# Optimization experiments

Measured on AMD Instinct MI355X. Metric: run time of the kernel, lower is better.

Reference implementation:

```python
import jax, jax.numpy as jnp
import numpy as np

RHO = 1.0
MU = 1e-05
DT = 1.0 / 32
DX = 1.0 / 255
DY = 1.0 / 255


def _residuals(x, std):
    # x: [B, 3, H, W]; torch does x *= std (pure version here)
    x = x * std
    u = x[:, 0]  # [B, H, W]
    v = x[:, 1]
    p = x[:, 2]
    r = jnp.roll

    dudt = (r(u, -1, 0) - r(u, 1, 0)) / DT
    dvdt = (r(v, -1, 0) - r(v, 1, 0)) / DT
    dudx = (r(u, -1, 1) - r(u, 1, 1)) / (2 * DX)
    dudy = (r(u, -1, 2) - r(u, 1, 2)) / (2 * DY)
    dvdx = (r(v, -1, 1) - r(v, 1, 1)) / (2 * DX)
    dvdy = (r(v, -1, 2) - r(v, 1, 2)) / (2 * DY)
    dpdx = (r(p, -1, 1) - r(p, 1, 1)) / (2 * DX)
    dpdy = (r(p, -1, 2) - r(p, 1, 2)) / (2 * DY)
    d2udx2 = (r(u, -1, 1) - 2 * u + r(u, 1, 1)) / DX ** 2
    d2udy2 = (r(u, -1, 2) - 2 * u + r(u, 1, 2)) / DY ** 2
    d2vdx2 = (r(v, -1, 1) - 2 * v + r(v, 1, 1)) / DX ** 2
    d2vdy2 = (r(v, -1, 2) - 2 * v + r(v, 1, 2)) / DY ** 2

    t = lambda a: a[1:-1, 1:-1, 1:-1]  # trim periodic-wrap halo
    u, v = t(u), t(v)
    r0 = jnp.abs(t(dudx) + t(dvdy))
    r1 = jnp.abs(RHO * (t(dudt) + u * t(dudx) + v * t(dudy)) + t(dpdx)
                 - MU * (t(d2udx2) + t(d2udy2)))
    r2 = jnp.abs(RHO * (t(dvdt) + u * t(dvdx) + v * t(dvdy)) + t(dpdy)
                 - MU * (t(d2vdx2) + t(d2vdy2)))
    return r0, r1, r2


def setup_inputs() -> dict:
    key = jax.random.key(0)
    k1, k2, k3 = jax.random.split(key, 3)
    B, C, H, W = 64, 3, 512, 512
    x = jax.random.normal(k1, (B, C, H, W), dtype=jnp.float32)
    y = jax.random.normal(k2, (B, C, H, W), dtype=jnp.float32)
    std = jax.random.uniform(k3, (), dtype=jnp.float32)
    return {"x": x, "y": y, "std": std}


def reference(x, y, std):
    r0_y, r1_y, r2_y = _residuals(y, std)
    r0_x, r1_x, r2_x = _residuals(x, std)
    d0 = jnp.mean((r0_y - r0_x) ** 2)
    d1 = jnp.mean((r1_y - r1_x) ** 2)
    d2 = jnp.mean((r2_y - r2_x) ** 2)
    return 0.001 * (d0 + d1 + d2)
```

## Files before the change

### kernel.cpp

```cpp
#include <hip/hip_runtime.h>


constexpr int Wd   = 512;
constexpr int CSTR = 512 * 512;
constexpr int BSTR = 3 * 512 * 512;

__device__ __forceinline__ float4 ld4(const float* p) {
    return *reinterpret_cast<const float4*>(p);
}
__device__ __forceinline__ float4 scale4(float4 a, float s) {
    return make_float4(a.x * s, a.y * s, a.z * s, a.w * s);
}

__device__ __forceinline__ void plane_resid(
    const float (&L)[3][4][256],
    int io, int jt, int jl,
    float4 eu, float4 ev, float4 ep,
    float4 um, float4 uc, float4 un,
    float4 vm, float4 vc, float4 vn,
    float4 pc,
    float uL, float vL, float pL,
    float uR, float vR, float pR,
    float sdx,
    float r0[4], float r1[4], float r2[4])
{
    float4 uxm, vxm, pxm, uxp, vxp, pxp;
    if (io == 0) { uxm = eu; vxm = ev; pxm = ep; }
    else {
        uxm = ld4(&L[0][io - 1][jl]);
        vxm = ld4(&L[1][io - 1][jl]);
        pxm = ld4(&L[2][io - 1][jl]);
    }
    if (io == 3) { uxp = eu; vxp = ev; pxp = ep; }
    else {
        uxp = ld4(&L[0][io + 1][jl]);
        vxp = ld4(&L[1][io + 1][jl]);
        pxp = ld4(&L[2][io + 1][jl]);
    }

    float u_l = __shfl_up(uc.w, 1);
    float v_l = __shfl_up(vc.w, 1);
    float p_l = __shfl_up(pc.w, 1);
    float u_r = __shfl_down(uc.x, 1);
    float v_r = __shfl_down(vc.x, 1);
    float p_r = __shfl_down(pc.x, 1);
    if (jt == 0)  { u_l = uL; v_l = vL; p_l = pL; }
    if (jt == 63) { u_r = uR; v_r = vR; p_r = pR; }

    const float ucA[4] = {uc.x, uc.y, uc.z, uc.w};
    const float vcA[4] = {vc.x, vc.y, vc.z, vc.w};
    const float umA[4] = {um.x, um.y, um.z, um.w};
    const float vmA[4] = {vm.x, vm.y, vm.z, vm.w};
    const float unA[4] = {un.x, un.y, un.z, un.w};
    const float vnA[4] = {vn.x, vn.y, vn.z, vn.w};
    const float ul[4]  = {u_l, uc.x, uc.y, uc.z};
    const float ur[4]  = {uc.y, uc.z, uc.w, u_r};
    const float vl[4]  = {v_l, vc.x, vc.y, vc.z};
    const float vr[4]  = {vc.y, vc.z, vc.w, v_r};
    const float pl[4]  = {p_l, pc.x, pc.y, pc.z};
    const float pr[4]  = {pc.y, pc.z, pc.w, p_r};
    const float uxpA[4] = {uxp.x, uxp.y, uxp.z, uxp.w};
    const float uxmA[4] = {uxm.x, uxm.y, uxm.z, uxm.w};
    const float vxpA[4] = {vxp.x, vxp.y, vxp.z, vxp.w};
    const float vxmA[4] = {vxm.x, vxm.y, vxm.z, vxm.w};
    const float pxpA[4] = {pxp.x, pxp.y, pxp.z, pxp.w};
    const float pxmA[4] = {pxm.x, pxm.y, pxm.z, pxm.w};

    #pragma unroll
    for (int k = 0; k < 4; ++k) {
        const float dudx = (uxpA[k] - uxmA[k]) * 127.5f;
        const float dvdx = (vxpA[k] - vxmA[k]) * 127.5f;
        const float dpdx = (pxpA[k] - pxmA[k]) * sdx;
        const float dudy = (ur[k] - ul[k]) * 127.5f;
        const float dvdy = (vr[k] - vl[k]) * 127.5f;
        const float dpdy = (pr[k] - pl[k]) * sdx;
        const float lapu = (uxpA[k] + uxmA[k] + ur[k] + ul[k]) * 0.65025f
                         - 2.601f * ucA[k];
        const float lapv = (vxpA[k] + vxmA[k] + vr[k] + vl[k]) * 0.65025f
                         - 2.601f * vcA[k];
        r0[k] = fabsf(dudx + dvdy);
        r1[k] = fabsf((unA[k] - umA[k]) * 32.0f + ucA[k] * dudx + vcA[k] * dudy
                      + dpdx - lapu);
        r2[k] = fabsf((vnA[k] - vmA[k]) * 32.0f + ucA[k] * dvdx + vcA[k] * dvdy
                      + dpdy - lapv);
    }
}

__global__ __launch_bounds__(256)
void ns_loss_kernel(const float* __restrict__ X, const float* __restrict__ Y,
                    const float* __restrict__ stdp, double* __restrict__ acc)
{
    __shared__ float lds[2][2][3][4][256];
    __shared__ float smr[3][4];

    const float s   = *stdp;
    const float sdx = s * 127.5f;

    const int orig = blockIdx.x;
    const int grp  = orig & 7;
    const int band = orig >> 3;
    const int z    = grp >> 1;
    const int jh   = grp & 1;

    const int tid = threadIdx.x;
    const int io  = tid >> 6;
    const int jt  = tid & 63;
    const int jl  = jt << 2;
    const int j0g = (jh << 8) + jl;
    const int irow = 1 + band * 4 + io;
    const int i    = min(irow, 511);
    const bool vrow = (irow <= 510);
    const int bs = 1 + 15 * z + (z == 3 ? 1 : 0);
    const int nsteps = (z < 2) ? 15 : 16;

    int c = bs * BSTR + i * Wd + j0g;
    const int eoff = (io == 0) ? -Wd : ((i < 511) ? Wd : 0);
    const bool isedge = (io == 0) || (io == 3);
    const int offL = (j0g == 0) ? 0 : -1;
    const int offR = (j0g == 508) ? 3 : 4;

    float4 xum = scale4(ld4(X + c - BSTR), s);
    float4 xuc = scale4(ld4(X + c), s);
    float4 xun = scale4(ld4(X + c + BSTR), s);
    float4 xvm = scale4(ld4(X + c - BSTR + CSTR), s);
    float4 xvc = scale4(ld4(X + c + CSTR), s);
    float4 xvn = scale4(ld4(X + c + BSTR + CSTR), s);
    float4 xpc = ld4(X + c + 2 * CSTR);
    float4 xpn = ld4(X + c + 2 * CSTR + BSTR);
    float4 yum = scale4(ld4(Y + c - BSTR), s);
    float4 yuc = scale4(ld4(Y + c), s);
    float4 yun = scale4(ld4(Y + c + BSTR), s);
    float4 yvm = scale4(ld4(Y + c - BSTR + CSTR), s);
    float4 yvc = scale4(ld4(Y + c + CSTR), s);
    float4 yvn = scale4(ld4(Y + c + BSTR + CSTR), s);
    float4 ypc = ld4(Y + c + 2 * CSTR);
    float4 ypn = ld4(Y + c + 2 * CSTR + BSTR);

    *(float4*)&lds[0][0][0][io][jl] = xuc;
    *(float4*)&lds[0][0][1][io][jl] = xvc;
    *(float4*)&lds[0][0][2][io][jl] = xpc;
    *(float4*)&lds[0][1][0][io][jl] = yuc;
    *(float4*)&lds[0][1][1][io][jl] = yvc;
    *(float4*)&lds[0][1][2][io][jl] = ypc;
    __syncthreads();

    float s0 = 0.0f, s1 = 0.0f, s2 = 0.0f;

    for (int k = 0; k < nsteps; ++k) {
        const int cur = k & 1;

        float4 xeu = make_float4(0, 0, 0, 0), xev = xeu, xep = xeu;
        float4 yeu = xeu, yev = xeu, yep = xeu;
        if (isedge) {
            xeu = scale4(ld4(X + c + eoff), s);
            xev = scale4(ld4(X + c + CSTR + eoff), s);
            xep = ld4(X + c + 2 * CSTR + eoff);
            yeu = scale4(ld4(Y + c + eoff), s);
            yev = scale4(ld4(Y + c + CSTR + eoff), s);
            yep = ld4(Y + c + 2 * CSTR + eoff);
        }
        float xuL = 0, xvL = 0, xpL = 0, yuL = 0, yvL = 0, ypL = 0;
        float xuR = 0, xvR = 0, xpR = 0, yuR = 0, yvR = 0, ypR = 0;
        if (jt == 0) {
            xuL = X[c + offL] * s; xvL = X[c + CSTR + offL] * s;
            xpL = X[c + 2 * CSTR + offL];
            yuL = Y[c + offL] * s; yvL = Y[c + CSTR + offL] * s;
            ypL = Y[c + 2 * CSTR + offL];
        }
        if (jt == 63) {
            xuR = X[c + offR] * s; xvR = X[c + CSTR + offR] * s;
            xpR = X[c + 2 * CSTR + offR];
            yuR = Y[c + offR] * s; yvR = Y[c + CSTR + offR] * s;
            ypR = Y[c + 2 * CSTR + offR];
        }

        float r0x[4], r1x[4], r2x[4], r0y[4], r1y[4], r2y[4];
        plane_resid(lds[cur][0], io, jt, jl, xeu, xev, xep,
                    xum, xuc, xun, xvm, xvc, xvn, xpc,
                    xuL, xvL, xpL, xuR, xvR, xpR, sdx, r0x, r1x, r2x);
        plane_resid(lds[cur][1], io, jt, jl, yeu, yev, yep,
                    yum, yuc, yun, yvm, yvc, yvn, ypc,
                    yuL, yvL, ypL, yuR, yvR, ypR, sdx, r0y, r1y, r2y);

        #pragma unroll
        for (int kk = 0; kk < 4; ++kk) {
            float e0 = r0y[kk] - r0x[kk];
            float e1 = r1y[kk] - r1x[kk];
            float e2 = r2y[kk] - r2x[kk];
            const bool dead = (!vrow) || (kk == 0 && j0g == 0)
                                      || (kk == 3 && j0g == 508);
            if (dead) { e0 = 0.0f; e1 = 0.0f; e2 = 0.0f; }
            s0 += e0 * e0; s1 += e1 * e1; s2 += e2 * e2;
        }

        *(float4*)&lds[cur ^ 1][0][0][io][jl] = xun;
        *(float4*)&lds[cur ^ 1][0][1][io][jl] = xvn;
        *(float4*)&lds[cur ^ 1][0][2][io][jl] = xpn;
        *(float4*)&lds[cur ^ 1][1][0][io][jl] = yun;
        *(float4*)&lds[cur ^ 1][1][1][io][jl] = yvn;
        *(float4*)&lds[cur ^ 1][1][2][io][jl] = ypn;

        const int pfo = (k + 1 < nsteps) ? 2 * BSTR : BSTR;
        const float4 xu2 = scale4(ld4(X + c + pfo), s);
        const float4 xv2 = scale4(ld4(X + c + pfo + CSTR), s);
        const float4 xp2 = ld4(X + c + pfo + 2 * CSTR);
        const float4 yu2 = scale4(ld4(Y + c + pfo), s);
        const float4 yv2 = scale4(ld4(Y + c + pfo + CSTR), s);
        const float4 yp2 = ld4(Y + c + pfo + 2 * CSTR);

        xum = xuc; xuc = xun; xun = xu2;
        xvm = xvc; xvc = xvn; xvn = xv2;
        xpc = xpn; xpn = xp2;
        yum = yuc; yuc = yun; yun = yu2;
        yvm = yvc; yvc = yvn; yvn = yv2;
        ypc = ypn; ypn = yp2;

        asm volatile("s_waitcnt lgkmcnt(0)" ::: "memory");
        __builtin_amdgcn_s_barrier();
        c += BSTR;
    }

    for (int o = 32; o > 0; o >>= 1) {
        s0 += __shfl_down(s0, o);
        s1 += __shfl_down(s1, o);
        s2 += __shfl_down(s2, o);
    }
    const int wid = tid >> 6;
    if (jt == 0) { smr[0][wid] = s0; smr[1][wid] = s1; smr[2][wid] = s2; }
    __syncthreads();
    if (tid == 0) {
        atomicAdd(&acc[0], (double)smr[0][0] + (double)smr[0][1]
                         + (double)smr[0][2] + (double)smr[0][3]);
        atomicAdd(&acc[1], (double)smr[1][0] + (double)smr[1][1]
                         + (double)smr[1][2] + (double)smr[1][3]);
        atomicAdd(&acc[2], (double)smr[2][0] + (double)smr[2][1]
                         + (double)smr[2][2] + (double)smr[2][3]);
    }
}

__global__ void ns_finalize_kernel(const double* __restrict__ acc,
                                   float* __restrict__ out)
{
    if (threadIdx.x == 0) {
        const double N = 62.0 * 510.0 * 510.0;
        out[0] = (float)(1.0e-3 * (acc[0] + acc[1] + acc[2]) / N);
    }
}

extern "C" void kernel_launch(void* const* d_in, const int* in_sizes, int n_in,
                              void* d_out, int out_size, void* d_ws, size_t ws_size,
                              hipStream_t stream) {
    const float* X    = (const float*)d_in[0];
    const float* Y    = (const float*)d_in[1];
    const float* stdp = (const float*)d_in[2];
    float* out  = (float*)d_out;
    double* acc = (double*)d_ws;

    hipMemsetAsync(acc, 0, 3 * sizeof(double), stream);

    dim3 block(256);
    dim3 grid(1024);
    ns_loss_kernel<<<grid, block, 0, stream>>>(X, Y, stdp, acc);
    ns_finalize_kernel<<<1, 64, 0, stream>>>(acc, out);
}
```

Baseline: 136.6 us.

## Split batch into five chunks, drop pressure LDS staging, remap block order

The grid grows from 1024 to 1280 blocks by cutting the batch dimension into five chunks of 12-13 steps instead of four chunks of 15-16. Block indices are remapped so that adjacent blocks cover different z chunks. The pressure channel is no longer staged in LDS; its row neighbours are read directly from global memory each step, which shrinks LDS and may raise occupancy. The shared reduction scratch now reuses the LDS buffer. The cost is more redundant halo loads per step, and the pressure neighbour loads may read one row before or after the valid rows on boundary bands.

```diff
diff --git a/kernel.cpp b/kernel.cpp
--- a/kernel.cpp
+++ b/kernel.cpp
@@ -13,29 +13,27 @@
 }
 
 __device__ __forceinline__ void plane_resid(
-    const float (&L)[3][4][256],
+    const float (&L)[2][4][256],
     int io, int jt, int jl,
-    float4 eu, float4 ev, float4 ep,
+    float4 eu, float4 ev,
     float4 um, float4 uc, float4 un,
     float4 vm, float4 vc, float4 vn,
-    float4 pc,
+    float4 pc, float4 pxp4, float4 pxm4,
     float uL, float vL, float pL,
     float uR, float vR, float pR,
     float sdx,
     float r0[4], float r1[4], float r2[4])
 {
-    float4 uxm, vxm, pxm, uxp, vxp, pxp;
-    if (io == 0) { uxm = eu; vxm = ev; pxm = ep; }
+    float4 uxm, vxm, uxp, vxp;
+    if (io == 0) { uxm = eu; vxm = ev; }
     else {
         uxm = ld4(&L[0][io - 1][jl]);
         vxm = ld4(&L[1][io - 1][jl]);
-        pxm = ld4(&L[2][io - 1][jl]);
-    }
-    if (io == 3) { uxp = eu; vxp = ev; pxp = ep; }
+    }
+    if (io == 3) { uxp = eu; vxp = ev; }
     else {
         uxp = ld4(&L[0][io + 1][jl]);
         vxp = ld4(&L[1][io + 1][jl]);
-        pxp = ld4(&L[2][io + 1][jl]);
     }
 
     float u_l = __shfl_up(uc.w, 1);
@@ -63,8 +61,8 @@
     const float uxmA[4] = {uxm.x, uxm.y, uxm.z, uxm.w};
     const float vxpA[4] = {vxp.x, vxp.y, vxp.z, vxp.w};
     const float vxmA[4] = {vxm.x, vxm.y, vxm.z, vxm.w};
-    const float pxpA[4] = {pxp.x, pxp.y, pxp.z, pxp.w};
-    const float pxmA[4] = {pxm.x, pxm.y, pxm.z, pxm.w};
+    const float pxpA[4] = {pxp4.x, pxp4.y, pxp4.z, pxp4.w};
+    const float pxmA[4] = {pxm4.x, pxm4.y, pxm4.z, pxm4.w};
 
     #pragma unroll
     for (int k = 0; k < 4; ++k) {
@@ -90,17 +88,17 @@
 void ns_loss_kernel(const float* __restrict__ X, const float* __restrict__ Y,
                     const float* __restrict__ stdp, double* __restrict__ acc)
 {
-    __shared__ float lds[2][2][3][4][256];
-    __shared__ float smr[3][4];
+    __shared__ float lds[2][2][2][4][256];
 
     const float s   = *stdp;
     const float sdx = s * 127.5f;
 
     const int orig = blockIdx.x;
-    const int grp  = orig & 7;
-    const int band = orig >> 3;
-    const int z    = grp >> 1;
-    const int jh   = grp & 1;
+    const int wg   = (orig & 7) * 160 + (orig >> 3);
+    const int z    = wg >> 8;
+    const int rem  = wg & 255;
+    const int jh   = rem >> 7;
+    const int band = rem & 127;
 
     const int tid = threadIdx.x;
     const int io  = tid >> 6;
@@ -110,8 +108,8 @@
     const int irow = 1 + band * 4 + io;
     const int i    = min(irow, 511);
     const bool vrow = (irow <= 510);
-    const int bs = 1 + 15 * z + (z == 3 ? 1 : 0);
-    const int nsteps = (z < 2) ? 15 : 16;
+    const int bs     = (z < 2) ? (1 + 13 * z) : (27 + 12 * (z - 2));
+    const int nsteps = (z < 2) ? 13 : 12;
 
     int c = bs * BSTR + i * Wd + j0g;
     const int eoff = (io == 0) ? -Wd : ((i < 511) ? Wd : 0);
@@ -126,7 +124,6 @@
     float4 xvc = scale4(ld4(X + c + CSTR), s);
     float4 xvn = scale4(ld4(X + c + BSTR + CSTR), s);
     float4 xpc = ld4(X + c + 2 * CSTR);
-    float4 xpn = ld4(X + c + 2 * CSTR + BSTR);
     float4 yum = scale4(ld4(Y + c - BSTR), s);
     float4 yuc = scale4(ld4(Y + c), s);
     float4 yun = scale4(ld4(Y + c + BSTR), s);
@@ -134,14 +131,13 @@
     float4 yvc = scale4(ld4(Y + c + CSTR), s);
     float4 yvn = scale4(ld4(Y + c + BSTR + CSTR), s);
     float4 ypc = ld4(Y + c + 2 * CSTR);
+    float4 xpn = ld4(X + c + 2 * CSTR + BSTR);
     float4 ypn = ld4(Y + c + 2 * CSTR + BSTR);
 
     *(float4*)&lds[0][0][0][io][jl] = xuc;
     *(float4*)&lds[0][0][1][io][jl] = xvc;
-    *(float4*)&lds[0][0][2][io][jl] = xpc;
     *(float4*)&lds[0][1][0][io][jl] = yuc;
     *(float4*)&lds[0][1][1][io][jl] = yvc;
-    *(float4*)&lds[0][1][2][io][jl] = ypc;
     __syncthreads();
 
     float s0 = 0.0f, s1 = 0.0f, s2 = 0.0f;
@@ -149,15 +145,17 @@
     for (int k = 0; k < nsteps; ++k) {
         const int cur = k & 1;
 
-        float4 xeu = make_float4(0, 0, 0, 0), xev = xeu, xep = xeu;
-        float4 yeu = xeu, yev = xeu, yep = xeu;
+        const float4 xpxp = ld4(X + c + 2 * CSTR + Wd);
+        const float4 xpxm = ld4(X + c + 2 * CSTR - Wd);
+        const float4 ypxp = ld4(Y + c + 2 * CSTR + Wd);
+        const float4 ypxm = ld4(Y + c + 2 * CSTR - Wd);
+        float4 xeu = make_float4(0, 0, 0, 0), xev = xeu;
+        float4 yeu = xeu, yev = xeu;
         if (isedge) {
             xeu = scale4(ld4(X + c + eoff), s);
             xev = scale4(ld4(X + c + CSTR + eoff), s);
-            xep = ld4(X + c + 2 * CSTR + eoff);
             yeu = scale4(ld4(Y + c + eoff), s);
             yev = scale4(ld4(Y + c + CSTR + eoff), s);
-            yep = ld4(Y + c + 2 * CSTR + eoff);
         }
         float xuL = 0, xvL = 0, xpL = 0, yuL = 0, yvL = 0, ypL = 0;
         float xuR = 0, xvR = 0, xpR = 0, yuR = 0, yvR = 0, ypR = 0;
@@ -175,11 +173,11 @@
         }
 
         float r0x[4], r1x[4], r2x[4], r0y[4], r1y[4], r2y[4];
-        plane_resid(lds[cur][0], io, jt, jl, xeu, xev, xep,
-                    xum, xuc, xun, xvm, xvc, xvn, xpc,
+        plane_resid(lds[cur][0], io, jt, jl, xeu, xev,
+                    xum, xuc, xun, xvm, xvc, xvn, xpc, xpxp, xpxm,
                     xuL, xvL, xpL, xuR, xvR, xpR, sdx, r0x, r1x, r2x);
-        plane_resid(lds[cur][1], io, jt, jl, yeu, yev, yep,
-                    yum, yuc, yun, yvm, yvc, yvn, ypc,
+        plane_resid(lds[cur][1], io, jt, jl, yeu, yev,
+                    yum, yuc, yun, yvm, yvc, yvn, ypc, ypxp, ypxm,
                     yuL, yvL, ypL, yuR, yvR, ypR, sdx, r0y, r1y, r2y);
 
         #pragma unroll
@@ -195,10 +193,8 @@
 
         *(float4*)&lds[cur ^ 1][0][0][io][jl] = xun;
         *(float4*)&lds[cur ^ 1][0][1][io][jl] = xvn;
-        *(float4*)&lds[cur ^ 1][0][2][io][jl] = xpn;
         *(float4*)&lds[cur ^ 1][1][0][io][jl] = yun;
         *(float4*)&lds[cur ^ 1][1][1][io][jl] = yvn;
-        *(float4*)&lds[cur ^ 1][1][2][io][jl] = ypn;
 
         const int pfo = (k + 1 < nsteps) ? 2 * BSTR : BSTR;
         const float4 xu2 = scale4(ld4(X + c + pfo), s);
@@ -225,16 +221,17 @@
         s1 += __shfl_down(s1, o);
         s2 += __shfl_down(s2, o);
     }
+    float* red = &lds[0][0][0][0][0];
     const int wid = tid >> 6;
-    if (jt == 0) { smr[0][wid] = s0; smr[1][wid] = s1; smr[2][wid] = s2; }
+    if (jt == 0) { red[wid] = s0; red[4 + wid] = s1; red[8 + wid] = s2; }
     __syncthreads();
     if (tid == 0) {
-        atomicAdd(&acc[0], (double)smr[0][0] + (double)smr[0][1]
-                         + (double)smr[0][2] + (double)smr[0][3]);
-        atomicAdd(&acc[1], (double)smr[1][0] + (double)smr[1][1]
-                         + (double)smr[1][2] + (double)smr[1][3]);
-        atomicAdd(&acc[2], (double)smr[2][0] + (double)smr[2][1]
-                         + (double)smr[2][2] + (double)smr[2][3]);
+        atomicAdd(&acc[0], (double)red[0] + (double)red[1]
+                         + (double)red[2] + (double)red[3]);
+        atomicAdd(&acc[1], (double)red[4] + (double)red[5]
+                         + (double)red[6] + (double)red[7]);
+        atomicAdd(&acc[2], (double)red[8] + (double)red[9]
+                         + (double)red[10] + (double)red[11]);
     }
 }
 
@@ -259,7 +256,7 @@
     hipMemsetAsync(acc, 0, 3 * sizeof(double), stream);
 
     dim3 block(256);
-    dim3 grid(1024);
+    dim3 grid(1280);
     ns_loss_kernel<<<grid, block, 0, stream>>>(X, Y, stdp, acc);
     ns_finalize_kernel<<<1, 64, 0, stream>>>(acc, out);
 }
```

New measurement: 161.8 us. +18.5%, slower.

## Split X and Y residual work across two thread groups in 512-thread blocks

Applied to the files above, without the earlier changes.

Doubles the block to 512 threads so one half computes residuals for X and the other for Y, with the X residuals exchanged through shared memory for the squared-difference sum. Each thread now holds roughly half the register state, which is meant to raise occupancy and memory-level parallelism. The one-step-ahead register prefetch with a double-buffered LDS stage is replaced by a single stage buffer loaded inside the loop, and a second barrier per step is added for the exchange. This risks exposing more load latency and adds synchronisation overhead.

```diff
diff --git a/kernel.cpp b/kernel.cpp
--- a/kernel.cpp
+++ b/kernel.cpp
@@ -86,11 +86,12 @@
     }
 }
 
-__global__ __launch_bounds__(256)
+__global__ __launch_bounds__(512)
 void ns_loss_kernel(const float* __restrict__ X, const float* __restrict__ Y,
                     const float* __restrict__ stdp, double* __restrict__ acc)
 {
-    __shared__ float lds[2][2][3][4][256];
+    __shared__ float stage[2][3][4][256];
+    __shared__ float rxch[3][4][256];
     __shared__ float smr[3][4];
 
     const float s   = *stdp;
@@ -103,8 +104,10 @@
     const int jh   = grp & 1;
 
     const int tid = threadIdx.x;
-    const int io  = tid >> 6;
-    const int jt  = tid & 63;
+    const int tg  = tid >> 8;
+    const int t8  = tid & 255;
+    const int io  = t8 >> 6;
+    const int jt  = t8 & 63;
     const int jl  = jt << 2;
     const int j0g = (jh << 8) + jl;
     const int irow = 1 + band * 4 + io;
@@ -113,120 +116,91 @@
     const int bs = 1 + 15 * z + (z == 3 ? 1 : 0);
     const int nsteps = (z < 2) ? 15 : 16;
 
+    const float* __restrict__ T = tg ? Y : X;
     int c = bs * BSTR + i * Wd + j0g;
     const int eoff = (io == 0) ? -Wd : ((i < 511) ? Wd : 0);
     const bool isedge = (io == 0) || (io == 3);
     const int offL = (j0g == 0) ? 0 : -1;
     const int offR = (j0g == 508) ? 3 : 4;
 
-    float4 xum = scale4(ld4(X + c - BSTR), s);
-    float4 xuc = scale4(ld4(X + c), s);
-    float4 xun = scale4(ld4(X + c + BSTR), s);
-    float4 xvm = scale4(ld4(X + c - BSTR + CSTR), s);
-    float4 xvc = scale4(ld4(X + c + CSTR), s);
-    float4 xvn = scale4(ld4(X + c + BSTR + CSTR), s);
-    float4 xpc = ld4(X + c + 2 * CSTR);
-    float4 xpn = ld4(X + c + 2 * CSTR + BSTR);
-    float4 yum = scale4(ld4(Y + c - BSTR), s);
-    float4 yuc = scale4(ld4(Y + c), s);
-    float4 yun = scale4(ld4(Y + c + BSTR), s);
-    float4 yvm = scale4(ld4(Y + c - BSTR + CSTR), s);
-    float4 yvc = scale4(ld4(Y + c + CSTR), s);
-    float4 yvn = scale4(ld4(Y + c + BSTR + CSTR), s);
-    float4 ypc = ld4(Y + c + 2 * CSTR);
-    float4 ypn = ld4(Y + c + 2 * CSTR + BSTR);
-
-    *(float4*)&lds[0][0][0][io][jl] = xuc;
-    *(float4*)&lds[0][0][1][io][jl] = xvc;
-    *(float4*)&lds[0][0][2][io][jl] = xpc;
-    *(float4*)&lds[0][1][0][io][jl] = yuc;
-    *(float4*)&lds[0][1][1][io][jl] = yvc;
-    *(float4*)&lds[0][1][2][io][jl] = ypc;
-    __syncthreads();
+    float4 um = scale4(ld4(T + c - BSTR), s);
+    float4 uc = scale4(ld4(T + c), s);
+    float4 vm = scale4(ld4(T + c - BSTR + CSTR), s);
+    float4 vc = scale4(ld4(T + c + CSTR), s);
+    float4 pc = ld4(T + c + 2 * CSTR);
 
     float s0 = 0.0f, s1 = 0.0f, s2 = 0.0f;
 
     for (int k = 0; k < nsteps; ++k) {
-        const int cur = k & 1;
-
-        float4 xeu = make_float4(0, 0, 0, 0), xev = xeu, xep = xeu;
-        float4 yeu = xeu, yev = xeu, yep = xeu;
+        const float4 unr = ld4(T + c + BSTR);
+        const float4 vnr = ld4(T + c + BSTR + CSTR);
+        const float4 pn  = ld4(T + c + BSTR + 2 * CSTR);
+        float4 eu = uc, ev = vc, ep = pc;
         if (isedge) {
-            xeu = scale4(ld4(X + c + eoff), s);
-            xev = scale4(ld4(X + c + CSTR + eoff), s);
-            xep = ld4(X + c + 2 * CSTR + eoff);
-            yeu = scale4(ld4(Y + c + eoff), s);
-            yev = scale4(ld4(Y + c + CSTR + eoff), s);
-            yep = ld4(Y + c + 2 * CSTR + eoff);
-        }
-        float xuL = 0, xvL = 0, xpL = 0, yuL = 0, yvL = 0, ypL = 0;
-        float xuR = 0, xvR = 0, xpR = 0, yuR = 0, yvR = 0, ypR = 0;
+            eu = scale4(ld4(T + c + eoff), s);
+            ev = scale4(ld4(T + c + CSTR + eoff), s);
+            ep = ld4(T + c + 2 * CSTR + eoff);
+        }
+        float uL = 0, vL = 0, pL = 0, uR = 0, vR = 0, pR = 0;
         if (jt == 0) {
-            xuL = X[c + offL] * s; xvL = X[c + CSTR + offL] * s;
-            xpL = X[c + 2 * CSTR + offL];
-            yuL = Y[c + offL] * s; yvL = Y[c + CSTR + offL] * s;
-            ypL = Y[c + 2 * CSTR + offL];
+            uL = T[c + offL] * s; vL = T[c + CSTR + offL] * s;
+            pL = T[c + 2 * CSTR + offL];
         }
         if (jt == 63) {
-            xuR = X[c + offR] * s; xvR = X[c + CSTR + offR] * s;
-            xpR = X[c + 2 * CSTR + offR];
-            yuR = Y[c + offR] * s; yvR = Y[c + CSTR + offR] * s;
-            ypR = Y[c + 2 * CSTR + offR];
-        }
-
-        float r0x[4], r1x[4], r2x[4], r0y[4], r1y[4], r2y[4];
-        plane_resid(lds[cur][0], io, jt, jl, xeu, xev, xep,
-                    xum, xuc, xun, xvm, xvc, xvn, xpc,
-                    xuL, xvL, xpL, xuR, xvR, xpR, sdx, r0x, r1x, r2x);
-        plane_resid(lds[cur][1], io, jt, jl, yeu, yev, yep,
-                    yum, yuc, yun, yvm, yvc, yvn, ypc,
-                    yuL, yvL, ypL, yuR, yvR, ypR, sdx, r0y, r1y, r2y);
-
-        #pragma unroll
-        for (int kk = 0; kk < 4; ++kk) {
-            float e0 = r0y[kk] - r0x[kk];
-            float e1 = r1y[kk] - r1x[kk];
-            float e2 = r2y[kk] - r2x[kk];
-            const bool dead = (!vrow) || (kk == 0 && j0g == 0)
-                                      || (kk == 3 && j0g == 508);
-            if (dead) { e0 = 0.0f; e1 = 0.0f; e2 = 0.0f; }
-            s0 += e0 * e0; s1 += e1 * e1; s2 += e2 * e2;
-        }
-
-        *(float4*)&lds[cur ^ 1][0][0][io][jl] = xun;
-        *(float4*)&lds[cur ^ 1][0][1][io][jl] = xvn;
-        *(float4*)&lds[cur ^ 1][0][2][io][jl] = xpn;
-        *(float4*)&lds[cur ^ 1][1][0][io][jl] = yun;
-        *(float4*)&lds[cur ^ 1][1][1][io][jl] = yvn;
-        *(float4*)&lds[cur ^ 1][1][2][io][jl] = ypn;
-
-        const int pfo = (k + 1 < nsteps) ? 2 * BSTR : BSTR;
-        const float4 xu2 = scale4(ld4(X + c + pfo), s);
-        const float4 xv2 = scale4(ld4(X + c + pfo + CSTR), s);
-        const float4 xp2 = ld4(X + c + pfo + 2 * CSTR);
-        const float4 yu2 = scale4(ld4(Y + c + pfo), s);
-        const float4 yv2 = scale4(ld4(Y + c + pfo + CSTR), s);
-        const float4 yp2 = ld4(Y + c + pfo + 2 * CSTR);
-
-        xum = xuc; xuc = xun; xun = xu2;
-        xvm = xvc; xvc = xvn; xvn = xv2;
-        xpc = xpn; xpn = xp2;
-        yum = yuc; yuc = yun; yun = yu2;
-        yvm = yvc; yvc = yvn; yvn = yv2;
-        ypc = ypn; ypn = yp2;
-
+            uR = T[c + offR] * s; vR = T[c + CSTR + offR] * s;
+            pR = T[c + 2 * CSTR + offR];
+        }
+
+        *(float4*)&stage[tg][0][io][jl] = uc;
+        *(float4*)&stage[tg][1][io][jl] = vc;
+        *(float4*)&stage[tg][2][io][jl] = pc;
         asm volatile("s_waitcnt lgkmcnt(0)" ::: "memory");
         __builtin_amdgcn_s_barrier();
+
+        const float4 un = scale4(unr, s);
+        const float4 vn = scale4(vnr, s);
+
+        float r0[4], r1[4], r2[4];
+        plane_resid(stage[tg], io, jt, jl, eu, ev, ep,
+                    um, uc, un, vm, vc, vn, pc,
+                    uL, vL, pL, uR, vR, pR, sdx, r0, r1, r2);
+
+        if (tg == 0) {
+            #pragma unroll
+            for (int kk = 0; kk < 4; ++kk) {
+                rxch[0][io][jl + kk] = r0[kk];
+                rxch[1][io][jl + kk] = r1[kk];
+                rxch[2][io][jl + kk] = r2[kk];
+            }
+        }
+        asm volatile("s_waitcnt lgkmcnt(0)" ::: "memory");
+        __builtin_amdgcn_s_barrier();
+
+        if (tg == 1) {
+            #pragma unroll
+            for (int kk = 0; kk < 4; ++kk) {
+                float e0 = r0[kk] - rxch[0][io][jl + kk];
+                float e1 = r1[kk] - rxch[1][io][jl + kk];
+                float e2 = r2[kk] - rxch[2][io][jl + kk];
+                const bool dead = (!vrow) || (kk == 0 && j0g == 0)
+                                          || (kk == 3 && j0g == 508);
+                if (dead) { e0 = 0.0f; e1 = 0.0f; e2 = 0.0f; }
+                s0 += e0 * e0; s1 += e1 * e1; s2 += e2 * e2;
+            }
+        }
+
+        um = uc; uc = un; vm = vc; vc = vn; pc = pn;
         c += BSTR;
     }
 
-    for (int o = 32; o > 0; o >>= 1) {
-        s0 += __shfl_down(s0, o);
-        s1 += __shfl_down(s1, o);
-        s2 += __shfl_down(s2, o);
-    }
-    const int wid = tid >> 6;
-    if (jt == 0) { smr[0][wid] = s0; smr[1][wid] = s1; smr[2][wid] = s2; }
+    if (tg == 1) {
+        for (int o = 32; o > 0; o >>= 1) {
+            s0 += __shfl_down(s0, o);
+            s1 += __shfl_down(s1, o);
+            s2 += __shfl_down(s2, o);
+        }
+        if (jt == 0) { smr[0][io] = s0; smr[1][io] = s1; smr[2][io] = s2; }
+    }
     __syncthreads();
     if (tid == 0) {
         atomicAdd(&acc[0], (double)smr[0][0] + (double)smr[0][1]
@@ -258,7 +232,7 @@
 
     hipMemsetAsync(acc, 0, 3 * sizeof(double), stream);
 
-    dim3 block(256);
+    dim3 block(512);
     dim3 grid(1024);
     ns_loss_kernel<<<grid, block, 0, stream>>>(X, Y, stdp, acc);
     ns_finalize_kernel<<<1, 64, 0, stream>>>(acc, out);
```

New measurement: 140.6 us. 3.0% more time.
